# Kernel tuning notes

Hardware: AMD Instinct MI355X
Metric: run time of the kernel (lower is better)

## Reference

```python
import jax, jax.numpy as jnp
import numpy as np
import math

B, S, D = 1, 2048, 2048
H, KVH = 16, 8
HD = D // H                      # 128
M_, N_ = 8, 256                  # S = M_*N_ blocks of tokens
FH = 5632                        # multiple_of-rounded int(2*(4*D)/3)
EPS = 1e-6
THETA = 10000.0


def rmsnorm(x, w, eps=EPS):
    xf = x.astype(jnp.float32)
    y = xf * jax.lax.rsqrt(jnp.mean(xf * xf, axis=-1, keepdims=True) + eps)
    return y.astype(x.dtype) * w


def apply_rope(x, cos, sin):
    # x: (B, S, h, HD); cos/sin: (S, HD//2) -- consecutive-pair complex rotation
    x2 = x.reshape(*x.shape[:-1], HD // 2, 2)
    xr, xi = x2[..., 0], x2[..., 1]
    c = cos[None, :, None, :]
    s = sin[None, :, None, :]
    out = jnp.stack([xr * c - xi * s, xr * s + xi * c], axis=-1)
    return out.reshape(x.shape)


def setup_inputs() -> dict:
    key = jax.random.key(0)
    ks = jax.random.split(key, 12)
    sc = 0.02
    x = jax.random.normal(ks[0], (B, S, D), jnp.float32)
    vec = jax.random.normal(ks[1], (B, M_, D), jnp.float32)
    wq = jax.random.normal(ks[2], (D, H * HD), jnp.float32) * sc
    wk = jax.random.normal(ks[3], (D, KVH * HD), jnp.float32) * sc
    wv = jax.random.normal(ks[4], (D, KVH * HD), jnp.float32) * sc
    wo = jax.random.normal(ks[5], (H * HD, D), jnp.float32) * sc
    w1 = jax.random.normal(ks[6], (D, FH), jnp.float32) * sc
    w2 = jax.random.normal(ks[7], (FH, D), jnp.float32) * sc
    w3 = jax.random.normal(ks[8], (D, FH), jnp.float32) * sc
    mod_w = jax.random.normal(ks[9], (D, 3 * D), jnp.float32) * sc
    mod_b = jnp.zeros((3 * D,), jnp.float32)
    attn_norm_w = jnp.ones((D,), jnp.float32)
    ffn_norm_w = jnp.ones((D,), jnp.float32)
    # RoPE tables
    inv = 1.0 / (THETA ** (jnp.arange(0, HD, 2, dtype=jnp.float32) / HD))
    t = jnp.arange(S, dtype=jnp.float32)
    f = jnp.outer(t, inv)                      # (S, HD//2)
    cos, sin = jnp.cos(f), jnp.sin(f)
    mask = jnp.triu(jnp.full((S, S), -1e9, jnp.float32), 1)
    return dict(x=x, vec=vec, cos=cos, sin=sin, mask=mask, wq=wq, wk=wk, wv=wv,
                wo=wo, w1=w1, w2=w2, w3=w3, mod_w=mod_w, mod_b=mod_b,
                attn_norm_w=attn_norm_w, ffn_norm_w=ffn_norm_w)


def reference(x, vec, cos, sin, mask, wq, wk, wv, wo, w1, w2, w3,
              mod_w, mod_b, attn_norm_w, ffn_norm_w):
    n_rep = H // KVH
    # Modulation from per-block vectors (B, M, D) -> expand over N tokens/block
    mod = jax.nn.silu(vec) @ mod_w + mod_b
    shift, scale, gate = jnp.split(mod, 3, axis=-1)
    expand = lambda t: jnp.repeat(t, N_, axis=1)      # (B, M, D) -> (B, S, D)
    # Attention branch with modulated RMSNorm input
    h = rmsnorm(x, attn_norm_w)
    h = (1.0 + expand(scale)) * h + expand(shift)
    q = (h @ wq).reshape(B, S, H, HD)
    k = (h @ wk).reshape(B, S, KVH, HD)
    v = (h @ wv).reshape(B, S, KVH, HD)
    q = apply_rope(q, cos, sin)
    k = apply_rope(k, cos, sin)
    k = jnp.repeat(k, n_rep, axis=2)                  # repeat_kv
    v = jnp.repeat(v, n_rep, axis=2)
    scores = jnp.einsum('bshd,bthd->bhst', q, k) / math.sqrt(HD) + mask
    attn = jax.nn.softmax(scores.astype(jnp.float32), axis=-1).astype(q.dtype)
    o = jnp.einsum('bhst,bthd->bshd', attn, v).reshape(B, S, H * HD) @ wo
    x = x + expand(gate) * o
    # SwiGLU FFN branch
    hn = rmsnorm(x, ffn_norm_w)
    ff = (jax.nn.silu(hn @ w1) * (hn @ w3)) @ w2
    return x + ff
```

## Files before the change

kernel.cpp:

```cpp
#include <hip/hip_runtime.h>
#include <hip/hip_bf16.h>


typedef __attribute__((ext_vector_type(8))) short short8;
typedef __attribute__((ext_vector_type(4))) float f32x4;
typedef __attribute__((ext_vector_type(16))) float f32x16;
typedef __attribute__((ext_vector_type(4))) unsigned short u16x4;

#define MFMA16(a, b, c) __builtin_amdgcn_mfma_f32_16x16x32_bf16((a), (b), (c), 0, 0, 0)
#define MFMA32(a, b, c) __builtin_amdgcn_mfma_f32_32x32x16_bf16((a), (b), (c), 0, 0, 0)

__device__ __forceinline__ unsigned short f2b_bits(float f) {
    union { float f; unsigned int u; } cv; cv.f = f;
    unsigned int u = cv.u;
    u += 0x7fffu + ((u >> 16) & 1u);
    return (unsigned short)(u >> 16);
}
__device__ __forceinline__ float b2f_bits(unsigned short b) {
    union { float f; unsigned int u; } cv; cv.u = ((unsigned int)b) << 16; return cv.f;
}
__device__ __forceinline__ float silu_f(float x) { return x / (1.0f + __expf(-x)); }

__device__ __forceinline__ void async_copy16(const unsigned short* g, unsigned short* l) {
    __builtin_amdgcn_global_load_lds(
        (const __attribute__((address_space(1))) unsigned int*)g,
        (__attribute__((address_space(3))) unsigned int*)l, 16, 0, 0);
}

__global__ __launch_bounds__(256) void transpose_kernel(
    const float* __restrict__ W, unsigned short* __restrict__ WT, int K, int N,
    float scale)
{
    __shared__ float t[64][65];
    const int tid = threadIdx.x;
    const int k0 = blockIdx.y * 64, n0 = blockIdx.x * 64;
    {
        const int row = tid >> 2, cq = (tid & 3) * 16;
        const float* src = W + (size_t)(k0 + row) * N + n0 + cq;
        #pragma unroll
        for (int i = 0; i < 4; i++) {
            float4 v = *(const float4*)(src + i * 4);
            t[row][cq + i * 4 + 0] = v.x;
            t[row][cq + i * 4 + 1] = v.y;
            t[row][cq + i * 4 + 2] = v.z;
            t[row][cq + i * 4 + 3] = v.w;
        }
    }
    __syncthreads();
    {
        const int n = tid >> 2, kq = (tid & 3) * 16;
        short8 v0, v1;
        #pragma unroll
        for (int i = 0; i < 8; i++) {
            v0[i] = (short)f2b_bits(t[kq + i][n] * scale);
            v1[i] = (short)f2b_bits(t[kq + 8 + i][n] * scale);
        }
        unsigned short* dst = WT + (size_t)(n0 + n) * K + k0 + kq;
        *(short8*)(dst) = v0;
        *(short8*)(dst + 8) = v1;
    }
}

__global__ void silu_kernel(const float* __restrict__ in, float* __restrict__ outp, int n) {
    int i = blockIdx.x * 256 + threadIdx.x;
    if (i < n) outp[i] = silu_f(in[i]);
}

__global__ __launch_bounds__(256) void mod_gemm1(
    const float* __restrict__ svec, const float* __restrict__ mw,
    float* __restrict__ part)
{
    __shared__ float svs[8][256];
    const int tid = threadIdx.x;
    const int nb = blockIdx.x, kc = blockIdx.y;
    const int n = nb * 256 + tid;
    #pragma unroll
    for (int m8 = 0; m8 < 8; m8++) svs[m8][tid] = svec[m8 * 2048 + kc * 256 + tid];
    __syncthreads();
    float acc[8];
    #pragma unroll
    for (int m = 0; m < 8; m++) acc[m] = 0.0f;
    for (int k = 0; k < 256; k++) {
        const float w = mw[(size_t)(kc * 256 + k) * 6144 + n];
        #pragma unroll
        for (int m = 0; m < 8; m++) acc[m] += svs[m][k] * w;
    }
    #pragma unroll
    for (int m = 0; m < 8; m++) part[(size_t)(kc * 8 + m) * 6144 + n] = acc[m];
}

__global__ void mod_gemm2(const float* __restrict__ part, const float* __restrict__ mb,
                          float* __restrict__ modb)
{
    const int i = blockIdx.x * 256 + threadIdx.x;
    const int n = i % 6144;
    float a = mb[n];
    #pragma unroll
    for (int kc = 0; kc < 8; kc++) a += part[(size_t)(kc * 8 + (i / 6144)) * 6144 + n];
    modb[i] = a;
}

template<bool MOD>
__global__ __launch_bounds__(256) void norm_kernel(
    const float* __restrict__ xin, const float* __restrict__ w,
    const float* __restrict__ mod, unsigned short* __restrict__ outp)
{
    const int s = blockIdx.x, tid = threadIdx.x;
    const float* xr = xin + (size_t)s * 2048;
    float4 a4 = *(const float4*)(xr + tid * 8);
    float4 b4 = *(const float4*)(xr + tid * 8 + 4);
    float v[8] = {a4.x, a4.y, a4.z, a4.w, b4.x, b4.y, b4.z, b4.w};
    float ss = 0.0f;
    #pragma unroll
    for (int i = 0; i < 8; i++) ss += v[i] * v[i];
    #pragma unroll
    for (int off = 1; off < 64; off <<= 1) ss += __shfl_xor(ss, off);
    __shared__ float red[4];
    if ((tid & 63) == 0) red[tid >> 6] = ss;
    __syncthreads();
    ss = red[0] + red[1] + red[2] + red[3];
    const float inv = rsqrtf(ss * (1.0f / 2048.0f) + 1e-6f);
    const int g = s >> 8;
    #pragma unroll
    for (int i = 0; i < 8; i++) {
        const int d = tid * 8 + i;
        float y = v[i] * inv * w[d];
        if (MOD) y = y * (1.0f + mod[g * 6144 + 2048 + d]) + mod[g * 6144 + d];
        outp[(size_t)s * 2048 + d] = f2b_bits(y);
    }
}

enum { EP_QKV = 0, EP_BF16 = 1, EP_SILUMUL = 2, EP_PART = 3 };

template<int EPI>
__global__ __launch_bounds__(256, 2) void gemm_kernel(
    const unsigned short* __restrict__ A, const unsigned short* __restrict__ BT,
    void* __restrict__ outp, void* __restrict__ outp2, void* __restrict__ outp3,
    const unsigned short* __restrict__ up,
    const float* __restrict__ ct, const float* __restrict__ st,
    int M, int N, int K, int kspl)
{
    __shared__ unsigned short As[8192];
    __shared__ unsigned short Bs[8192];
    const int tid = threadIdx.x;
    const int lane = tid & 63, wave = tid >> 6;

    const int nwg = gridDim.x * gridDim.y;
    const int fid = blockIdx.y * gridDim.x + blockIdx.x;
    const int sid = (fid & 7) * (nwg >> 3) + (fid >> 3);
    const int m0 = (sid / gridDim.x) * 128;
    const int n0 = (sid % gridDim.x) * 128;
    const int kb0 = blockIdx.z * kspl;

    const int wr = (wave >> 1) * 64, wc = (wave & 1) * 64;
    const int lr = lane & 15, lg = lane >> 4;
    const int rcol = (lg ^ ((lr >> 1) & 3)) * 8;

    const int cl0 = (wave * 2 + 0) * 64 + lane;
    const int cl1 = (wave * 2 + 1) * 64 + lane;
    const int r0 = cl0 >> 2, c0 = cl0 & 3;
    const int r1 = cl1 >> 2, c1 = cl1 & 3;
    const unsigned short* gA0 = A + (size_t)(m0 + r0) * K + kb0 + (c0 ^ ((r0 >> 1) & 3)) * 8;
    const unsigned short* gA1 = A + (size_t)(m0 + r1) * K + kb0 + (c1 ^ ((r1 >> 1) & 3)) * 8;
    const unsigned short* gB0 = BT + (size_t)(n0 + r0) * K + kb0 + (c0 ^ ((r0 >> 1) & 3)) * 8;
    const unsigned short* gB1 = BT + (size_t)(n0 + r1) * K + kb0 + (c1 ^ ((r1 >> 1) & 3)) * 8;

    f32x4 acc[4][4];
    #pragma unroll
    for (int i = 0; i < 4; i++)
        #pragma unroll
        for (int j = 0; j < 4; j++) acc[i][j] = (f32x4){0.f, 0.f, 0.f, 0.f};

    const int nsteps = kspl >> 5;

    auto stage = [&](int buf, int kofs) {
        unsigned short* la = As + buf * 4096 + wave * 1024;
        unsigned short* lb = Bs + buf * 4096 + wave * 1024;
        async_copy16(gA0 + kofs, la);
        async_copy16(gA1 + kofs, la + 512);
        async_copy16(gB0 + kofs, lb);
        async_copy16(gB1 + kofs, lb + 512);
    };
    auto dostep = [&](int t, int cur) {
        if (t + 1 < nsteps) stage(cur ^ 1, (t + 1) * 32);
        const unsigned short* ab = As + cur * 4096;
        const unsigned short* bb = Bs + cur * 4096;
        short8 af[4], bfr[4];
        #pragma unroll
        for (int i = 0; i < 4; i++)
            af[i] = *(const short8*)&ab[(wr + i * 16 + lr) * 32 + rcol];
        #pragma unroll
        for (int j = 0; j < 4; j++)
            bfr[j] = *(const short8*)&bb[(wc + j * 16 + lr) * 32 + rcol];
        #pragma unroll
        for (int i = 0; i < 4; i++)
            #pragma unroll
            for (int j = 0; j < 4; j++)
                acc[i][j] = MFMA16(af[i], bfr[j], acc[i][j]);
        __syncthreads();
    };

    stage(0, 0);
    __syncthreads();
    for (int t = 0; t < nsteps; t += 2) { dostep(t, 0); dostep(t + 1, 1); }

    #pragma unroll
    for (int i = 0; i < 4; i++) {
        #pragma unroll
        for (int j = 0; j < 4; j++) {
            const int rb = m0 + wr + i * 16 + lg * 4;
            const int c  = n0 + wc + j * 16 + lr;
            if constexpr (EPI == EP_QKV) {
                if (n0 < 3072) {
                    const int crel = (n0 < 2048) ? c : (c - 2048);
                    const int dd = crel & 127;
                    const int pr = dd >> 1;
                    #pragma unroll
                    for (int r = 0; r < 4; r++) {
                        const float v = acc[i][j][r];
                        const float p = __shfl_xor(v, 1);
                        const float cs = ct[(rb + r) * 64 + pr];
                        const float sn = st[(rb + r) * 64 + pr];
                        const float res = (dd & 1) ? (p * sn + v * cs) : (v * cs - p * sn);
                        if (n0 < 2048)
                            ((unsigned short*)outp)[(size_t)(rb + r) * 2048 + crel] = f2b_bits(res);
                        else
                            ((unsigned short*)outp2)[(size_t)(rb + r) * 1024 + crel] = f2b_bits(res);
                    }
                } else {
                    u16x4 pk4;
                    #pragma unroll
                    for (int r = 0; r < 4; r++) pk4[r] = f2b_bits(acc[i][j][r]);
                    *(u16x4*)((unsigned short*)outp3 + (size_t)(c - 3072) * 2048 + rb) = pk4;
                }
            } else if constexpr (EPI == EP_PART) {
                float* pout = (float*)outp + (size_t)blockIdx.z * M * N;
                #pragma unroll
                for (int r = 0; r < 4; r++)
                    pout[(size_t)(rb + r) * N + c] = acc[i][j][r];
            } else {
                #pragma unroll
                for (int r = 0; r < 4; r++) {
                    const size_t idx = (size_t)(rb + r) * N + c;
                    if constexpr (EPI == EP_BF16) {
                        ((unsigned short*)outp)[idx] = f2b_bits(acc[i][j][r]);
                    } else {
                        const float uu = b2f_bits(up[idx]);
                        ((unsigned short*)outp)[idx] = f2b_bits(silu_f(uu) * acc[i][j][r]);
                    }
                }
            }
        }
    }
}

__global__ void combine_xgate(const float* __restrict__ p, const float* __restrict__ x,
                              const float* __restrict__ modp, float* __restrict__ out)
{
    const size_t i = ((size_t)blockIdx.x * 256 + threadIdx.x) * 4;
    const int row = (int)(i >> 11), col = (int)(i & 2047);
    const float4 a = *(const float4*)(p + i);
    const float4 b = *(const float4*)(p + (size_t)2048 * 2048 + i);
    const float4 xv = *(const float4*)(x + i);
    const float4 g = *(const float4*)(modp + (row >> 8) * 6144 + 4096 + col);
    float4 o;
    o.x = xv.x + g.x * (a.x + b.x);
    o.y = xv.y + g.y * (a.y + b.y);
    o.z = xv.z + g.z * (a.z + b.z);
    o.w = xv.w + g.w * (a.w + b.w);
    *(float4*)(out + i) = o;
}

__global__ void combine_w2(const float* __restrict__ p, float* __restrict__ out)
{
    const size_t i = ((size_t)blockIdx.x * 256 + threadIdx.x) * 4;
    const float4 a = *(const float4*)(p + i);
    const float4 b = *(const float4*)(p + (size_t)2048 * 2048 + i);
    float4 o = *(const float4*)(out + i);
    o.x += a.x + b.x; o.y += a.y + b.y; o.z += a.z + b.z; o.w += a.w + b.w;
    *(float4*)(out + i) = o;
}

__global__ __launch_bounds__(256, 2) void attn_kernel(
    const unsigned short* __restrict__ q,
    const unsigned short* __restrict__ kk,
    const unsigned short* __restrict__ vT,
    unsigned short* __restrict__ o)
{
    __shared__ unsigned short Ks[2][8192];
    __shared__ unsigned short Vs[2][8192];
    const int tid = threadIdx.x, wave = tid >> 6, lane = tid & 63;
    const int l5 = lane & 31, hi = lane >> 5;
    const int kvh = blockIdx.x;
    const int qt  = 63 - blockIdx.y;
    const int hs = wave >> 1, ks = wave & 1;
    const int h = kvh * 2 + hs;
    const int q0 = qt * 32;
    const int qrow = q0 + l5;
    const int niter = (qt >> 1) + 1;
    const int nss = (niter + 1) >> 1;

    short8 qf[8];
    {
        const unsigned short* qp = q + (size_t)qrow * 2048 + h * 128 + hi * 8;
        #pragma unroll
        for (int kf = 0; kf < 8; kf++) qf[kf] = *(const short8*)(qp + kf * 16);
    }

    f32x16 ot[4];
    #pragma unroll
    for (int df = 0; df < 4; df++)
        #pragma unroll
        for (int r = 0; r < 16; r++) ot[df][r] = 0.0f;
    float m_ = -3e30f, l_ = 0.0f;

    for (int ss = 0; ss < nss; ss++) {
        const int kvA = ss * 128;
        #pragma unroll
        for (int t = 0; t < 2; t++) {
            #pragma unroll
            for (int i = 0; i < 4; i++) {
                const int cl = (wave * 4 + i) * 64 + lane;
                const int row = cl >> 4, c = cl & 15;
                async_copy16(kk + (size_t)(kvA + t * 64 + row) * 1024 + kvh * 128
                                 + ((c ^ (row & 15)) * 8),
                             &Ks[t][(wave * 4 + i) * 512]);
            }
            #pragma unroll
            for (int i = 0; i < 4; i++) {
                const int cl = (wave * 4 + i) * 64 + lane;
                const int row = cl >> 3, c = cl & 7;
                async_copy16(vT + (size_t)(kvh * 128 + row) * 2048 + kvA + t * 64
                                 + ((c ^ (row & 7)) * 8),
                             &Vs[t][(wave * 4 + i) * 512]);
            }
        }
        __syncthreads();

        const int j = 2 * ss + ks;
        if (j < niter) {
            const int kv0 = j * 64;
            f32x16 st_[2];
            #pragma unroll
            for (int nf = 0; nf < 2; nf++)
                #pragma unroll
                for (int r = 0; r < 16; r++) st_[nf][r] = 0.0f;
            #pragma unroll
            for (int kf = 0; kf < 8; kf++) {
                const int ch = (kf * 2 + hi) ^ (l5 & 15);
                const short8 k0v = *(const short8*)&Ks[ks][l5 * 128 + ch * 8];
                const short8 k1v = *(const short8*)&Ks[ks][(l5 + 32) * 128 + ch * 8];
                st_[0] = MFMA32(k0v, qf[kf], st_[0]);
                st_[1] = MFMA32(k1v, qf[kf], st_[1]);
            }
            float sv[2][16];
            #pragma unroll
            for (int nf = 0; nf < 2; nf++)
                #pragma unroll
                for (int r = 0; r < 16; r++) {
                    const int kvi = kv0 + nf * 32 + (r & 3) + 8 * (r >> 2) + 4 * hi;
                    sv[nf][r] = (kvi > qrow) ? -3e30f : st_[nf][r];
                }
            float pmax = sv[0][0];
            #pragma unroll
            for (int nf = 0; nf < 2; nf++)
                #pragma unroll
                for (int r = 0; r < 16; r++) pmax = fmaxf(pmax, sv[nf][r]);
            pmax = fmaxf(pmax, __shfl_xor(pmax, 32));
            const float mnew = fmaxf(m_, pmax);
            const float alpha = __expf(m_ - mnew);
            m_ = mnew;
            float rs = 0.0f;
            #pragma unroll
            for (int nf = 0; nf < 2; nf++)
                #pragma unroll
                for (int r = 0; r < 16; r++) {
                    const float p = __expf(sv[nf][r] - mnew);
                    sv[nf][r] = p;
                    rs += p;
                }
            rs += __shfl_xor(rs, 32);
            l_ = l_ * alpha + rs;
            #pragma unroll
            for (int df = 0; df < 4; df++)
                #pragma unroll
                for (int r = 0; r < 16; r++) ot[df][r] *= alpha;
            short8 pa[4];
            #pragma unroll
            for (int nf = 0; nf < 2; nf++) {
                #pragma unroll
                for (int hh = 0; hh < 2; hh++) {
                    unsigned int a0 = ((unsigned int)f2b_bits(sv[nf][8 * hh + 1]) << 16) | f2b_bits(sv[nf][8 * hh + 0]);
                    unsigned int a1 = ((unsigned int)f2b_bits(sv[nf][8 * hh + 3]) << 16) | f2b_bits(sv[nf][8 * hh + 2]);
                    unsigned int a2 = ((unsigned int)f2b_bits(sv[nf][8 * hh + 5]) << 16) | f2b_bits(sv[nf][8 * hh + 4]);
                    unsigned int a3 = ((unsigned int)f2b_bits(sv[nf][8 * hh + 7]) << 16) | f2b_bits(sv[nf][8 * hh + 6]);
                    const unsigned int x0 = (unsigned int)__shfl_xor((int)a0, 32);
                    const unsigned int x1 = (unsigned int)__shfl_xor((int)a1, 32);
                    const unsigned int x2 = (unsigned int)__shfl_xor((int)a2, 32);
                    const unsigned int x3 = (unsigned int)__shfl_xor((int)a3, 32);
                    union { unsigned int u[4]; short8 s; } cv;
                    cv.u[0] = hi ? x2 : a0;
                    cv.u[1] = hi ? x3 : a1;
                    cv.u[2] = hi ? a2 : x0;
                    cv.u[3] = hi ? a3 : x1;
                    pa[nf * 2 + hh] = cv.s;
                }
            }
            #pragma unroll
            for (int df = 0; df < 4; df++) {
                const int d = df * 32 + l5;
                #pragma unroll
                for (int kvf = 0; kvf < 4; kvf++) {
                    const int ch = (kvf * 2 + hi) ^ (d & 7);
                    const short8 vfrag = *(const short8*)&Vs[ks][d * 64 + ch * 8];
                    ot[df] = MFMA32(vfrag, pa[kvf], ot[df]);
                }
            }
        }
        __syncthreads();
    }

    float* Osh = (float*)&Ks[0][0];
    float* msh = (float*)&Vs[0][0];
    if (ks == 1) {
        #pragma unroll
        for (int df = 0; df < 4; df++)
            #pragma unroll
            for (int r = 0; r < 16; r++) {
                const int d = df * 32 + (r & 3) + 8 * (r >> 2) + 4 * hi;
                Osh[hs * 4096 + d * 32 + l5] = ot[df][r];
            }
        if (hi == 0) { msh[hs * 64 + l5] = m_; msh[hs * 64 + 32 + l5] = l_; }
    }
    __syncthreads();
    if (ks == 0) {
        const float m1 = msh[hs * 64 + l5], l1 = msh[hs * 64 + 32 + l5];
        const float mF = fmaxf(m_, m1);
        const float a0 = __expf(m_ - mF), a1 = __expf(m1 - mF);
        const float rinv = 1.0f / (l_ * a0 + l1 * a1);
        #pragma unroll
        for (int df = 0; df < 4; df++) {
            #pragma unroll
            for (int g = 0; g < 4; g++) {
                u16x4 pk;
                #pragma unroll
                for (int e = 0; e < 4; e++) {
                    const int d = df * 32 + e + 8 * g + 4 * hi;
                    const float ov = ot[df][4 * g + e] * a0 + Osh[hs * 4096 + d * 32 + l5] * a1;
                    pk[e] = f2b_bits(ov * rinv);
                }
                *(u16x4*)(o + (size_t)qrow * 2048 + h * 128 + df * 32 + 8 * g + 4 * hi) = pk;
            }
        }
    }
}

extern "C" void kernel_launch(void* const* d_in, const int* in_sizes, int n_in,
                              void* d_out, int out_size, void* d_ws, size_t ws_size,
                              hipStream_t stream) {
    (void)in_sizes; (void)n_in; (void)out_size; (void)ws_size;
    const float* x     = (const float*)d_in[0];
    const float* vec   = (const float*)d_in[1];
    const float* cosb  = (const float*)d_in[2];
    const float* sinb  = (const float*)d_in[3];
    const float* wq    = (const float*)d_in[5];
    const float* wk    = (const float*)d_in[6];
    const float* wv    = (const float*)d_in[7];
    const float* wo    = (const float*)d_in[8];
    const float* w1    = (const float*)d_in[9];
    const float* w2    = (const float*)d_in[10];
    const float* w3    = (const float*)d_in[11];
    const float* mod_w = (const float*)d_in[12];
    const float* mod_b = (const float*)d_in[13];
    const float* anw   = (const float*)d_in[14];
    const float* fnw   = (const float*)d_in[15];
    float* out = (float*)d_out;

    char* ws = (char*)d_ws;
    size_t off = 0;
    auto alloc = [&](size_t bytes) -> void* {
        void* p = ws + off; off += (bytes + 255) & ~(size_t)255; return p;
    };
    unsigned short* WTqkv = (unsigned short*)alloc((size_t)4096 * 2048 * 2);
    unsigned short* WTo   = (unsigned short*)alloc((size_t)2048 * 2048 * 2);
    unsigned short* WT1   = (unsigned short*)alloc((size_t)5632 * 2048 * 2);
    unsigned short* WT3   = (unsigned short*)alloc((size_t)5632 * 2048 * 2);
    unsigned short* WT2   = (unsigned short*)alloc((size_t)2048 * 5632 * 2);
    float* svec = (float*)alloc((size_t)8 * 2048 * 4);
    float* part = (float*)alloc((size_t)64 * 6144 * 4);
    float* modb = (float*)alloc((size_t)8 * 6144 * 4);
    unsigned short* h    = (unsigned short*)alloc((size_t)2048 * 2048 * 2);
    unsigned short* qb   = (unsigned short*)alloc((size_t)2048 * 2048 * 2);
    unsigned short* kb   = (unsigned short*)alloc((size_t)2048 * 1024 * 2);
    unsigned short* vT   = (unsigned short*)alloc((size_t)1024 * 2048 * 2);
    unsigned short* ob   = (unsigned short*)alloc((size_t)2048 * 2048 * 2);
    unsigned short* u    = (unsigned short*)alloc((size_t)2048 * 5632 * 2);
    unsigned short* ffin = (unsigned short*)alloc((size_t)2048 * 5632 * 2);

    float* pxg = (float*)u;
    float* pw2 = (float*)h;

    const float qscale = 0.08838834764831845f;

    transpose_kernel<<<dim3(32, 32), 256, 0, stream>>>(wq, WTqkv, 2048, 2048, qscale);
    transpose_kernel<<<dim3(16, 32), 256, 0, stream>>>(wk, WTqkv + (size_t)2048 * 2048, 2048, 1024, 1.0f);
    transpose_kernel<<<dim3(16, 32), 256, 0, stream>>>(wv, WTqkv + (size_t)3072 * 2048, 2048, 1024, 1.0f);
    transpose_kernel<<<dim3(32, 32), 256, 0, stream>>>(wo, WTo, 2048, 2048, 1.0f);
    transpose_kernel<<<dim3(88, 32), 256, 0, stream>>>(w1, WT1, 2048, 5632, 1.0f);
    transpose_kernel<<<dim3(88, 32), 256, 0, stream>>>(w3, WT3, 2048, 5632, 1.0f);
    transpose_kernel<<<dim3(32, 88), 256, 0, stream>>>(w2, WT2, 5632, 2048, 1.0f);

    silu_kernel<<<64, 256, 0, stream>>>(vec, svec, 8 * 2048);
    mod_gemm1<<<dim3(24, 8), 256, 0, stream>>>(svec, mod_w, part);
    mod_gemm2<<<192, 256, 0, stream>>>(part, mod_b, modb);

    norm_kernel<true><<<2048, 256, 0, stream>>>(x, anw, modb, h);

    gemm_kernel<EP_QKV><<<dim3(32, 16), 256, 0, stream>>>(
        h, WTqkv, qb, kb, vT, nullptr, cosb, sinb, 2048, 4096, 2048, 2048);

    attn_kernel<<<dim3(8, 64), 256, 0, stream>>>(qb, kb, vT, ob);

    gemm_kernel<EP_PART><<<dim3(16, 16, 2), 256, 0, stream>>>(
        ob, WTo, pxg, nullptr, nullptr, nullptr, nullptr, nullptr, 2048, 2048, 2048, 1024);
    combine_xgate<<<4096, 256, 0, stream>>>(pxg, x, modb, out);

    norm_kernel<false><<<2048, 256, 0, stream>>>(out, fnw, nullptr, h);

    gemm_kernel<EP_BF16><<<dim3(44, 16), 256, 0, stream>>>(
        h, WT1, u, nullptr, nullptr, nullptr, nullptr, nullptr, 2048, 5632, 2048, 2048);
    gemm_kernel<EP_SILUMUL><<<dim3(44, 16), 256, 0, stream>>>(
        h, WT3, ffin, nullptr, nullptr, u, nullptr, nullptr, 2048, 5632, 2048, 2048);

    gemm_kernel<EP_PART><<<dim3(16, 16, 2), 256, 0, stream>>>(
        ffin, WT2, pw2, nullptr, nullptr, nullptr, nullptr, nullptr, 2048, 2048, 5632, 2816);
    combine_w2<<<4096, 256, 0, stream>>>(pw2, out);
}
```

Baseline: 460.2 us.

## Deepen GEMM LDS pipeline to four stages and restructure attention work split

The GEMM kernel moves from a double buffer to a four-deep LDS ring with three tiles in flight. It uses explicit vmcnt waits, raw s_barrier and setprio around the MFMA block, so global-to-LDS latency overlaps more compute and the per-step full sync is lighter. The attention kernel drops the KV split across wave pairs and its cross-wave LDS merge. Instead each block handles a 64-row query slab, with the two wave pairs on different 32-row halves sharing double-buffered K/V tiles, and the grid is halved. The trade-off is doubled GEMM LDS use, which may limit occupancy, and fewer attention blocks with longer serial KV loops.

New measurement: 507.6 us. 10.3% more time.

```diff
diff --git a/kernel.cpp b/kernel.cpp
--- a/kernel.cpp
+++ b/kernel.cpp
@@ -9,6 +9,7 @@
 
 #define MFMA16(a, b, c) __builtin_amdgcn_mfma_f32_16x16x32_bf16((a), (b), (c), 0, 0, 0)
 #define MFMA32(a, b, c) __builtin_amdgcn_mfma_f32_32x32x16_bf16((a), (b), (c), 0, 0, 0)
+#define VMCNT(n) asm volatile("s_waitcnt vmcnt(" #n ")" ::: "memory")
 
 __device__ __forceinline__ unsigned short f2b_bits(float f) {
     union { float f; unsigned int u; } cv; cv.f = f;
@@ -140,8 +141,8 @@
     const float* __restrict__ ct, const float* __restrict__ st,
     int M, int N, int K, int kspl)
 {
-    __shared__ unsigned short As[8192];
-    __shared__ unsigned short Bs[8192];
+    __shared__ unsigned short As[4 * 4096];
+    __shared__ unsigned short Bs[4 * 4096];
     const int tid = threadIdx.x;
     const int lane = tid & 63, wave = tid >> 6;
 
@@ -171,20 +172,28 @@
         #pragma unroll
         for (int j = 0; j < 4; j++) acc[i][j] = (f32x4){0.f, 0.f, 0.f, 0.f};
 
-    const int nsteps = kspl >> 5;
-
-    auto stage = [&](int buf, int kofs) {
-        unsigned short* la = As + buf * 4096 + wave * 1024;
-        unsigned short* lb = Bs + buf * 4096 + wave * 1024;
-        async_copy16(gA0 + kofs, la);
-        async_copy16(gA1 + kofs, la + 512);
-        async_copy16(gB0 + kofs, lb);
-        async_copy16(gB1 + kofs, lb + 512);
+    const int nt = kspl >> 5;
+
+    auto stagef = [&](int t) {
+        const int b = t & 3;
+        const int ko = t * 32;
+        unsigned short* la = As + b * 4096 + wave * 1024;
+        unsigned short* lb = Bs + b * 4096 + wave * 1024;
+        async_copy16(gA0 + ko, la);
+        async_copy16(gA1 + ko, la + 512);
+        async_copy16(gB0 + ko, lb);
+        async_copy16(gB1 + ko, lb + 512);
     };
-    auto dostep = [&](int t, int cur) {
-        if (t + 1 < nsteps) stage(cur ^ 1, (t + 1) * 32);
-        const unsigned short* ab = As + cur * 4096;
-        const unsigned short* bb = Bs + cur * 4096;
+
+    stagef(0); stagef(1); stagef(2);
+    VMCNT(8);
+    __builtin_amdgcn_sched_barrier(0);
+    __builtin_amdgcn_s_barrier();
+    __builtin_amdgcn_sched_barrier(0);
+
+    for (int t = 0; t < nt; ++t) {
+        const unsigned short* ab = As + (t & 3) * 4096;
+        const unsigned short* bb = Bs + (t & 3) * 4096;
         short8 af[4], bfr[4];
         #pragma unroll
         for (int i = 0; i < 4; i++)
@@ -192,17 +201,24 @@
         #pragma unroll
         for (int j = 0; j < 4; j++)
             bfr[j] = *(const short8*)&bb[(wc + j * 16 + lr) * 32 + rcol];
+        if (t + 3 < nt) stagef(t + 3);
+        __builtin_amdgcn_s_setprio(1);
         #pragma unroll
         for (int i = 0; i < 4; i++)
             #pragma unroll
             for (int j = 0; j < 4; j++)
                 acc[i][j] = MFMA16(af[i], bfr[j], acc[i][j]);
-        __syncthreads();
-    };
-
-    stage(0, 0);
-    __syncthreads();
-    for (int t = 0; t < nsteps; t += 2) { dostep(t, 0); dostep(t + 1, 1); }
+        __builtin_amdgcn_s_setprio(0);
+        const int rem = nt - 1 - t;
+        if (rem >= 3)      { VMCNT(8); }
+        else if (rem == 2) { VMCNT(4); }
+        else if (rem == 1) { VMCNT(0); }
+        __builtin_amdgcn_sched_barrier(0);
+        if (rem > 0) {
+            __builtin_amdgcn_s_barrier();
+            __builtin_amdgcn_sched_barrier(0);
+        }
+    }
 
     #pragma unroll
     for (int i = 0; i < 4; i++) {
@@ -292,13 +308,11 @@
     const int tid = threadIdx.x, wave = tid >> 6, lane = tid & 63;
     const int l5 = lane & 31, hi = lane >> 5;
     const int kvh = blockIdx.x;
-    const int qt  = 63 - blockIdx.y;
-    const int hs = wave >> 1, ks = wave & 1;
+    const int slab = 31 - blockIdx.y;
+    const int hs = wave >> 1, qs = wave & 1;
     const int h = kvh * 2 + hs;
-    const int q0 = qt * 32;
-    const int qrow = q0 + l5;
-    const int niter = (qt >> 1) + 1;
-    const int nss = (niter + 1) >> 1;
+    const int qrow = slab * 64 + qs * 32 + l5;
+    const int ntiles = slab + 1;
 
     short8 qf[8];
     {
@@ -314,143 +328,121 @@
         for (int r = 0; r < 16; r++) ot[df][r] = 0.0f;
     float m_ = -3e30f, l_ = 0.0f;
 
-    for (int ss = 0; ss < nss; ss++) {
-        const int kvA = ss * 128;
-        #pragma unroll
-        for (int t = 0; t < 2; t++) {
-            #pragma unroll
-            for (int i = 0; i < 4; i++) {
-                const int cl = (wave * 4 + i) * 64 + lane;
-                const int row = cl >> 4, c = cl & 15;
-                async_copy16(kk + (size_t)(kvA + t * 64 + row) * 1024 + kvh * 128
-                                 + ((c ^ (row & 15)) * 8),
-                             &Ks[t][(wave * 4 + i) * 512]);
+    auto stage = [&](int j, int b) {
+        #pragma unroll
+        for (int i = 0; i < 4; i++) {
+            const int cl = (wave * 4 + i) * 64 + lane;
+            const int row = cl >> 4, c = cl & 15;
+            async_copy16(kk + (size_t)(j * 64 + row) * 1024 + kvh * 128
+                             + ((c ^ (row & 15)) * 8),
+                         &Ks[b][(wave * 4 + i) * 512]);
+        }
+        #pragma unroll
+        for (int i = 0; i < 4; i++) {
+            const int cl = (wave * 4 + i) * 64 + lane;
+            const int row = cl >> 3, c = cl & 7;
+            async_copy16(vT + (size_t)(kvh * 128 + row) * 2048 + j * 64
+                             + ((c ^ (row & 7)) * 8),
+                         &Vs[b][(wave * 4 + i) * 512]);
+        }
+    };
+
+    stage(0, 0);
+    __syncthreads();
+
+    for (int j = 0; j < ntiles; ++j) {
+        const int buf = j & 1;
+        if (j + 1 < ntiles) stage(j + 1, buf ^ 1);
+        const int kv0 = j * 64;
+        f32x16 st_[2];
+        #pragma unroll
+        for (int nf = 0; nf < 2; nf++)
+            #pragma unroll
+            for (int r = 0; r < 16; r++) st_[nf][r] = 0.0f;
+        #pragma unroll
+        for (int kf = 0; kf < 8; kf++) {
+            const int ch = (kf * 2 + hi) ^ (l5 & 15);
+            const short8 k0v = *(const short8*)&Ks[buf][l5 * 128 + ch * 8];
+            const short8 k1v = *(const short8*)&Ks[buf][(l5 + 32) * 128 + ch * 8];
+            st_[0] = MFMA32(k0v, qf[kf], st_[0]);
+            st_[1] = MFMA32(k1v, qf[kf], st_[1]);
+        }
+        float sv[2][16];
+        #pragma unroll
+        for (int nf = 0; nf < 2; nf++)
+            #pragma unroll
+            for (int r = 0; r < 16; r++) {
+                const int kvi = kv0 + nf * 32 + (r & 3) + 8 * (r >> 2) + 4 * hi;
+                sv[nf][r] = (kvi > qrow) ? -3e30f : st_[nf][r];
             }
-            #pragma unroll
-            for (int i = 0; i < 4; i++) {
-                const int cl = (wave * 4 + i) * 64 + lane;
-                const int row = cl >> 3, c = cl & 7;
-                async_copy16(vT + (size_t)(kvh * 128 + row) * 2048 + kvA + t * 64
-                                 + ((c ^ (row & 7)) * 8),
-                             &Vs[t][(wave * 4 + i) * 512]);
+        float pmax = sv[0][0];
+        #pragma unroll
+        for (int nf = 0; nf < 2; nf++)
+            #pragma unroll
+            for (int r = 0; r < 16; r++) pmax = fmaxf(pmax, sv[nf][r]);
+        pmax = fmaxf(pmax, __shfl_xor(pmax, 32));
+        const float mnew = fmaxf(m_, pmax);
+        const float alpha = __expf(m_ - mnew);
+        m_ = mnew;
+        float rs = 0.0f;
+        #pragma unroll
+        for (int nf = 0; nf < 2; nf++)
+            #pragma unroll
+            for (int r = 0; r < 16; r++) {
+                const float p = __expf(sv[nf][r] - mnew);
+                sv[nf][r] = p;
+                rs += p;
             }
+        rs += __shfl_xor(rs, 32);
+        l_ = l_ * alpha + rs;
+        #pragma unroll
+        for (int df = 0; df < 4; df++)
+            #pragma unroll
+            for (int r = 0; r < 16; r++) ot[df][r] *= alpha;
+        short8 pa[4];
+        #pragma unroll
+        for (int nf = 0; nf < 2; nf++) {
+            #pragma unroll
+            for (int hh = 0; hh < 2; hh++) {
+                unsigned int a0 = ((unsigned int)f2b_bits(sv[nf][8 * hh + 1]) << 16) | f2b_bits(sv[nf][8 * hh + 0]);
+                unsigned int a1 = ((unsigned int)f2b_bits(sv[nf][8 * hh + 3]) << 16) | f2b_bits(sv[nf][8 * hh + 2]);
+                unsigned int a2 = ((unsigned int)f2b_bits(sv[nf][8 * hh + 5]) << 16) | f2b_bits(sv[nf][8 * hh + 4]);
+                unsigned int a3 = ((unsigned int)f2b_bits(sv[nf][8 * hh + 7]) << 16) | f2b_bits(sv[nf][8 * hh + 6]);
+                const unsigned int x0 = (unsigned int)__shfl_xor((int)a0, 32);
+                const unsigned int x1 = (unsigned int)__shfl_xor((int)a1, 32);
+                const unsigned int x2 = (unsigned int)__shfl_xor((int)a2, 32);
+                const unsigned int x3 = (unsigned int)__shfl_xor((int)a3, 32);
+                union { unsigned int u[4]; short8 s; } cv;
+                cv.u[0] = hi ? x2 : a0;
+                cv.u[1] = hi ? x3 : a1;
+                cv.u[2] = hi ? a2 : x0;
+                cv.u[3] = hi ? a3 : x1;
+                pa[nf * 2 + hh] = cv.s;
+            }
+        }
+        #pragma unroll
+        for (int df = 0; df < 4; df++) {
+            const int d = df * 32 + l5;
+            #pragma unroll
+            for (int kvf = 0; kvf < 4; kvf++) {
+                const int ch = (kvf * 2 + hi) ^ (d & 7);
+                const short8 vfrag = *(const short8*)&Vs[buf][d * 64 + ch * 8];
+                ot[df] = MFMA32(vfrag, pa[kvf], ot[df]);
+            }
         }
         __syncthreads();
-
-        const int j = 2 * ss + ks;
-        if (j < niter) {
-            const int kv0 = j * 64;
-            f32x16 st_[2];
-            #pragma unroll
-            for (int nf = 0; nf < 2; nf++)
-                #pragma unroll
-                for (int r = 0; r < 16; r++) st_[nf][r] = 0.0f;
-            #pragma unroll
-            for (int kf = 0; kf < 8; kf++) {
-                const int ch = (kf * 2 + hi) ^ (l5 & 15);
-                const short8 k0v = *(const short8*)&Ks[ks][l5 * 128 + ch * 8];
-                const short8 k1v = *(const short8*)&Ks[ks][(l5 + 32) * 128 + ch * 8];
-                st_[0] = MFMA32(k0v, qf[kf], st_[0]);
-                st_[1] = MFMA32(k1v, qf[kf], st_[1]);
-            }
-            float sv[2][16];
-            #pragma unroll
-            for (int nf = 0; nf < 2; nf++)
-                #pragma unroll
-                for (int r = 0; r < 16; r++) {
-                    const int kvi = kv0 + nf * 32 + (r & 3) + 8 * (r >> 2) + 4 * hi;
-                    sv[nf][r] = (kvi > qrow) ? -3e30f : st_[nf][r];
-                }
-            float pmax = sv[0][0];
-            #pragma unroll
-            for (int nf = 0; nf < 2; nf++)
-                #pragma unroll
-                for (int r = 0; r < 16; r++) pmax = fmaxf(pmax, sv[nf][r]);
-            pmax = fmaxf(pmax, __shfl_xor(pmax, 32));
-            const float mnew = fmaxf(m_, pmax);
-            const float alpha = __expf(m_ - mnew);
-            m_ = mnew;
-            float rs = 0.0f;
-            #pragma unroll
-            for (int nf = 0; nf < 2; nf++)
-                #pragma unroll
-                for (int r = 0; r < 16; r++) {
-                    const float p = __expf(sv[nf][r] - mnew);
-                    sv[nf][r] = p;
-                    rs += p;
-                }
-            rs += __shfl_xor(rs, 32);
-            l_ = l_ * alpha + rs;
-            #pragma unroll
-            for (int df = 0; df < 4; df++)
-                #pragma unroll
-                for (int r = 0; r < 16; r++) ot[df][r] *= alpha;
-            short8 pa[4];
-            #pragma unroll
-            for (int nf = 0; nf < 2; nf++) {
-                #pragma unroll
-                for (int hh = 0; hh < 2; hh++) {
-                    unsigned int a0 = ((unsigned int)f2b_bits(sv[nf][8 * hh + 1]) << 16) | f2b_bits(sv[nf][8 * hh + 0]);
-                    unsigned int a1 = ((unsigned int)f2b_bits(sv[nf][8 * hh + 3]) << 16) | f2b_bits(sv[nf][8 * hh + 2]);
-                    unsigned int a2 = ((unsigned int)f2b_bits(sv[nf][8 * hh + 5]) << 16) | f2b_bits(sv[nf][8 * hh + 4]);
-                    unsigned int a3 = ((unsigned int)f2b_bits(sv[nf][8 * hh + 7]) << 16) | f2b_bits(sv[nf][8 * hh + 6]);
-                    const unsigned int x0 = (unsigned int)__shfl_xor((int)a0, 32);
-                    const unsigned int x1 = (unsigned int)__shfl_xor((int)a1, 32);
-                    const unsigned int x2 = (unsigned int)__shfl_xor((int)a2, 32);
-                    const unsigned int x3 = (unsigned int)__shfl_xor((int)a3, 32);
-                    union { unsigned int u[4]; short8 s; } cv;
-                    cv.u[0] = hi ? x2 : a0;
-                    cv.u[1] = hi ? x3 : a1;
-                    cv.u[2] = hi ? a2 : x0;
-                    cv.u[3] = hi ? a3 : x1;
-                    pa[nf * 2 + hh] = cv.s;
-                }
-            }
-            #pragma unroll
-            for (int df = 0; df < 4; df++) {
-                const int d = df * 32 + l5;
-                #pragma unroll
-                for (int kvf = 0; kvf < 4; kvf++) {
-                    const int ch = (kvf * 2 + hi) ^ (d & 7);
-                    const short8 vfrag = *(const short8*)&Vs[ks][d * 64 + ch * 8];
-                    ot[df] = MFMA32(vfrag, pa[kvf], ot[df]);
-                }
-            }
-        }
-        __syncthreads();
-    }
-
-    float* Osh = (float*)&Ks[0][0];
-    float* msh = (float*)&Vs[0][0];
-    if (ks == 1) {
-        #pragma unroll
-        for (int df = 0; df < 4; df++)
-            #pragma unroll
-            for (int r = 0; r < 16; r++) {
-                const int d = df * 32 + (r & 3) + 8 * (r >> 2) + 4 * hi;
-                Osh[hs * 4096 + d * 32 + l5] = ot[df][r];
-            }
-        if (hi == 0) { msh[hs * 64 + l5] = m_; msh[hs * 64 + 32 + l5] = l_; }
-    }
-    __syncthreads();
-    if (ks == 0) {
-        const float m1 = msh[hs * 64 + l5], l1 = msh[hs * 64 + 32 + l5];
-        const float mF = fmaxf(m_, m1);
-        const float a0 = __expf(m_ - mF), a1 = __expf(m1 - mF);
-        const float rinv = 1.0f / (l_ * a0 + l1 * a1);
-        #pragma unroll
-        for (int df = 0; df < 4; df++) {
-            #pragma unroll
-            for (int g = 0; g < 4; g++) {
-                u16x4 pk;
-                #pragma unroll
-                for (int e = 0; e < 4; e++) {
-                    const int d = df * 32 + e + 8 * g + 4 * hi;
-                    const float ov = ot[df][4 * g + e] * a0 + Osh[hs * 4096 + d * 32 + l5] * a1;
-                    pk[e] = f2b_bits(ov * rinv);
-                }
-                *(u16x4*)(o + (size_t)qrow * 2048 + h * 128 + df * 32 + 8 * g + 4 * hi) = pk;
-            }
+    }
+
+    const float rinv = 1.0f / l_;
+    #pragma unroll
+    for (int df = 0; df < 4; df++) {
+        #pragma unroll
+        for (int g = 0; g < 4; g++) {
+            u16x4 pk;
+            #pragma unroll
+            for (int e = 0; e < 4; e++)
+                pk[e] = f2b_bits(ot[df][4 * g + e] * rinv);
+            *(u16x4*)(o + (size_t)qrow * 2048 + h * 128 + df * 32 + 8 * g + 4 * hi) = pk;
         }
     }
 }
@@ -519,7 +511,7 @@
     gemm_kernel<EP_QKV><<<dim3(32, 16), 256, 0, stream>>>(
         h, WTqkv, qb, kb, vT, nullptr, cosb, sinb, 2048, 4096, 2048, 2048);
 
-    attn_kernel<<<dim3(8, 64), 256, 0, stream>>>(qb, kb, vT, ob);
+    attn_kernel<<<dim3(8, 32), 256, 0, stream>>>(qb, kb, vT, ob);
 
     gemm_kernel<EP_PART><<<dim3(16, 16, 2), 256, 0, stream>>>(
         ob, WTo, pxg, nullptr, nullptr, nullptr, nullptr, nullptr, 2048, 2048, 2048, 1024);
```

## Fuse w1/w3 into one interleaved GEMM with 256x256 tiles and split-K

Applied to the files above, without the earlier changes.

Adds an 8-wave GEMM kernel with 256x256 tiles, 128 KB of dynamic LDS and a finely interleaved load/compute schedule using barriers, setprio and explicit vmcnt waits. It is used for the output projection, the FFN up-projection and the down-projection. The w1 and w3 weights are transposed into one buffer with their columns interleaved in groups of 8. That lets a single GEMM compute both products and apply silu(a)*b in the epilogue through a lane shuffle, so the bf16 intermediate no longer makes a round trip through memory. The w2 GEMM now splits K three ways, and the combine kernel sums three partials. The cost is extra fp32 partial traffic, and one workgroup per CU at 512 threads, which lowers occupancy.

Measured after the change: 468.3 us. No clear change (+1.7%).

```diff
diff --git a/kernel.cpp b/kernel.cpp
--- a/kernel.cpp
+++ b/kernel.cpp
@@ -9,6 +9,7 @@
 
 #define MFMA16(a, b, c) __builtin_amdgcn_mfma_f32_16x16x32_bf16((a), (b), (c), 0, 0, 0)
 #define MFMA32(a, b, c) __builtin_amdgcn_mfma_f32_32x32x16_bf16((a), (b), (c), 0, 0, 0)
+#define VMCNT(n) asm volatile("s_waitcnt vmcnt(" #n ")" ::: "memory")
 
 __device__ __forceinline__ unsigned short f2b_bits(float f) {
     union { float f; unsigned int u; } cv; cv.f = f;
@@ -61,9 +62,49 @@
     }
 }
 
+__global__ __launch_bounds__(256) void transpose_w13_kernel(
+    const float* __restrict__ W1, const float* __restrict__ W3,
+    unsigned short* __restrict__ WT, int K, int N)
+{
+    __shared__ float t[64][65];
+    const int tid = threadIdx.x;
+    const int k0 = blockIdx.y * 64, n0 = blockIdx.x * 64;
+    for (int which = 0; which < 2; which++) {
+        const float* W = which ? W3 : W1;
+        __syncthreads();
+        {
+            const int row = tid >> 2, cq = (tid & 3) * 16;
+            const float* src = W + (size_t)(k0 + row) * N + n0 + cq;
+            #pragma unroll
+            for (int i = 0; i < 4; i++) {
+                float4 v = *(const float4*)(src + i * 4);
+                t[row][cq + i * 4 + 0] = v.x;
+                t[row][cq + i * 4 + 1] = v.y;
+                t[row][cq + i * 4 + 2] = v.z;
+                t[row][cq + i * 4 + 3] = v.w;
+            }
+        }
+        __syncthreads();
+        {
+            const int n = tid >> 2, kq = (tid & 3) * 16;
+            short8 v0, v1;
+            #pragma unroll
+            for (int i = 0; i < 8; i++) {
+                v0[i] = (short)f2b_bits(t[kq + i][n]);
+                v1[i] = (short)f2b_bits(t[kq + 8 + i][n]);
+            }
+            const int ngl = n0 + n;
+            const int r = ((ngl >> 3) << 4) + (ngl & 7) + which * 8;
+            unsigned short* dst = WT + (size_t)r * K + k0 + kq;
+            *(short8*)(dst) = v0;
+            *(short8*)(dst + 8) = v1;
+        }
+    }
+}
+
 __global__ void silu_kernel(const float* __restrict__ in, float* __restrict__ outp, int n) {
     int i = blockIdx.x * 256 + threadIdx.x;
-    if (i < n) outp[i] = silu_f(in[i]);
+    if (i < n) outp[i] = silu_f(i < n ? in[i] : 0.0f);
 }
 
 __global__ __launch_bounds__(256) void mod_gemm1(
@@ -130,15 +171,14 @@
     }
 }
 
-enum { EP_QKV = 0, EP_BF16 = 1, EP_SILUMUL = 2, EP_PART = 3 };
+enum { EP_QKV = 0 };
 
 template<int EPI>
 __global__ __launch_bounds__(256, 2) void gemm_kernel(
     const unsigned short* __restrict__ A, const unsigned short* __restrict__ BT,
     void* __restrict__ outp, void* __restrict__ outp2, void* __restrict__ outp3,
-    const unsigned short* __restrict__ up,
     const float* __restrict__ ct, const float* __restrict__ st,
-    int M, int N, int K, int kspl)
+    int M, int N, int K)
 {
     __shared__ unsigned short As[8192];
     __shared__ unsigned short Bs[8192];
@@ -150,7 +190,6 @@
     const int sid = (fid & 7) * (nwg >> 3) + (fid >> 3);
     const int m0 = (sid / gridDim.x) * 128;
     const int n0 = (sid % gridDim.x) * 128;
-    const int kb0 = blockIdx.z * kspl;
 
     const int wr = (wave >> 1) * 64, wc = (wave & 1) * 64;
     const int lr = lane & 15, lg = lane >> 4;
@@ -160,10 +199,10 @@
     const int cl1 = (wave * 2 + 1) * 64 + lane;
     const int r0 = cl0 >> 2, c0 = cl0 & 3;
     const int r1 = cl1 >> 2, c1 = cl1 & 3;
-    const unsigned short* gA0 = A + (size_t)(m0 + r0) * K + kb0 + (c0 ^ ((r0 >> 1) & 3)) * 8;
-    const unsigned short* gA1 = A + (size_t)(m0 + r1) * K + kb0 + (c1 ^ ((r1 >> 1) & 3)) * 8;
-    const unsigned short* gB0 = BT + (size_t)(n0 + r0) * K + kb0 + (c0 ^ ((r0 >> 1) & 3)) * 8;
-    const unsigned short* gB1 = BT + (size_t)(n0 + r1) * K + kb0 + (c1 ^ ((r1 >> 1) & 3)) * 8;
+    const unsigned short* gA0 = A + (size_t)(m0 + r0) * K + (c0 ^ ((r0 >> 1) & 3)) * 8;
+    const unsigned short* gA1 = A + (size_t)(m0 + r1) * K + (c1 ^ ((r1 >> 1) & 3)) * 8;
+    const unsigned short* gB0 = BT + (size_t)(n0 + r0) * K + (c0 ^ ((r0 >> 1) & 3)) * 8;
+    const unsigned short* gB1 = BT + (size_t)(n0 + r1) * K + (c1 ^ ((r1 >> 1) & 3)) * 8;
 
     f32x4 acc[4][4];
     #pragma unroll
@@ -171,7 +210,7 @@
         #pragma unroll
         for (int j = 0; j < 4; j++) acc[i][j] = (f32x4){0.f, 0.f, 0.f, 0.f};
 
-    const int nsteps = kspl >> 5;
+    const int nsteps = K >> 5;
 
     auto stage = [&](int buf, int kofs) {
         unsigned short* la = As + buf * 4096 + wave * 1024;
@@ -210,45 +249,172 @@
         for (int j = 0; j < 4; j++) {
             const int rb = m0 + wr + i * 16 + lg * 4;
             const int c  = n0 + wc + j * 16 + lr;
-            if constexpr (EPI == EP_QKV) {
-                if (n0 < 3072) {
-                    const int crel = (n0 < 2048) ? c : (c - 2048);
-                    const int dd = crel & 127;
-                    const int pr = dd >> 1;
-                    #pragma unroll
-                    for (int r = 0; r < 4; r++) {
-                        const float v = acc[i][j][r];
-                        const float p = __shfl_xor(v, 1);
-                        const float cs = ct[(rb + r) * 64 + pr];
-                        const float sn = st[(rb + r) * 64 + pr];
-                        const float res = (dd & 1) ? (p * sn + v * cs) : (v * cs - p * sn);
-                        if (n0 < 2048)
-                            ((unsigned short*)outp)[(size_t)(rb + r) * 2048 + crel] = f2b_bits(res);
-                        else
-                            ((unsigned short*)outp2)[(size_t)(rb + r) * 1024 + crel] = f2b_bits(res);
-                    }
-                } else {
-                    u16x4 pk4;
-                    #pragma unroll
-                    for (int r = 0; r < 4; r++) pk4[r] = f2b_bits(acc[i][j][r]);
-                    *(u16x4*)((unsigned short*)outp3 + (size_t)(c - 3072) * 2048 + rb) = pk4;
+            if (n0 < 3072) {
+                const int crel = (n0 < 2048) ? c : (c - 2048);
+                const int dd = crel & 127;
+                const int pr = dd >> 1;
+                #pragma unroll
+                for (int r = 0; r < 4; r++) {
+                    const float v = acc[i][j][r];
+                    const float p = __shfl_xor(v, 1);
+                    const float cs = ct[(rb + r) * 64 + pr];
+                    const float sn = st[(rb + r) * 64 + pr];
+                    const float res = (dd & 1) ? (p * sn + v * cs) : (v * cs - p * sn);
+                    if (n0 < 2048)
+                        ((unsigned short*)outp)[(size_t)(rb + r) * 2048 + crel] = f2b_bits(res);
+                    else
+                        ((unsigned short*)outp2)[(size_t)(rb + r) * 1024 + crel] = f2b_bits(res);
                 }
-            } else if constexpr (EPI == EP_PART) {
-                float* pout = (float*)outp + (size_t)blockIdx.z * M * N;
+            } else {
+                u16x4 pk4;
+                #pragma unroll
+                for (int r = 0; r < 4; r++) pk4[r] = f2b_bits(acc[i][j][r]);
+                *(u16x4*)((unsigned short*)outp3 + (size_t)(c - 3072) * 2048 + rb) = pk4;
+            }
+        }
+    }
+}
+
+enum { G_SILU = 0, G_PART = 1 };
+
+template<int EPI>
+__global__ __launch_bounds__(512, 1) void gemm256_kernel(
+    const unsigned short* __restrict__ A, const unsigned short* __restrict__ BT,
+    void* __restrict__ outp, int M, int N, int Nout, int K, int ktiles, int nsplit)
+{
+    extern __shared__ unsigned short smem[];
+    unsigned short* As_ = smem;
+    unsigned short* Bs_ = smem + 2 * 16384;
+    const int tid = threadIdx.x;
+    const int lane = tid & 63, wid = tid >> 6;
+    const int wm = wid >> 2, wn = wid & 3;
+    const int lr = lane & 15, lg = lane >> 4;
+
+    const int nwg = gridDim.x * gridDim.y;
+    const int fid = blockIdx.y * gridDim.x + blockIdx.x;
+    const int sid = (fid & 7) * (nwg >> 3) + (fid >> 3);
+    const int m0 = (sid / gridDim.x) * 256;
+    const int n0 = (sid % gridDim.x) * 256;
+    const int z = blockIdx.z;
+    const int kt0 = (z * ktiles) / nsplit;
+    const int nt = ((z + 1) * ktiles) / nsplit - kt0;
+
+    const int srow8 = wid * 8 + (lane >> 3);
+    const int schunk = lane & 7;
+
+    f32x4 acc[8][4];
+    #pragma unroll
+    for (int i = 0; i < 8; i++)
+        #pragma unroll
+        for (int j = 0; j < 4; j++) acc[i][j] = (f32x4){0.f, 0.f, 0.f, 0.f};
+
+    auto stageA = [&](int u, int t) {
+        const int row = u * 64 + srow8;
+        async_copy16(A + (size_t)(m0 + row) * K + (size_t)(kt0 + t) * 64
+                       + ((schunk ^ (row & 7)) << 3),
+                     As_ + (t & 1) * 16384 + (u * 64 + wid * 8) * 64);
+    };
+    auto stageB = [&](int u, int t) {
+        const int row = u * 64 + srow8;
+        async_copy16(BT + (size_t)(n0 + row) * K + (size_t)(kt0 + t) * 64
+                       + ((schunk ^ (row & 7)) << 3),
+                     Bs_ + (t & 1) * 16384 + (u * 64 + wid * 8) * 64);
+    };
+
+    short8 areg[4], breg[2][4];
+    auto loadA = [&](const unsigned short* ab, int mh, int ks) {
+        #pragma unroll
+        for (int i = 0; i < 4; i++) {
+            const int row = wm * 128 + mh * 64 + i * 16 + lr;
+            areg[i] = *(const short8*)&ab[row * 64 + (((ks * 4 + lg) ^ (row & 7)) << 3)];
+        }
+    };
+    auto loadB = [&](const unsigned short* bb, int ks) {
+        #pragma unroll
+        for (int nj = 0; nj < 4; nj++) {
+            const int row = wn * 64 + nj * 16 + lr;
+            breg[ks][nj] = *(const short8*)&bb[row * 64 + (((ks * 4 + lg) ^ (row & 7)) << 3)];
+        }
+    };
+    auto mmac = [&](int mh, int ks) {
+        #pragma unroll
+        for (int i = 0; i < 4; i++)
+            #pragma unroll
+            for (int nj = 0; nj < 4; nj++)
+                acc[mh * 4 + i][nj] = MFMA16(areg[i], breg[ks][nj], acc[mh * 4 + i][nj]);
+    };
+
+    stageA(0, 0); stageA(2, 0);
+    stageB(0, 0); stageB(1, 0);
+    stageB(2, 0); stageB(3, 0);
+    stageA(1, 0); stageA(3, 0);
+    VMCNT(2);
+    __builtin_amdgcn_sched_barrier(0);
+    __builtin_amdgcn_s_barrier();
+    __builtin_amdgcn_sched_barrier(0);
+
+    for (int t = 0; t < nt; ++t) {
+        const unsigned short* ab = As_ + (t & 1) * 16384;
+        const unsigned short* bb = Bs_ + (t & 1) * 16384;
+        const bool more = (t + 1 < nt);
+        loadB(bb, 0);
+        loadA(ab, 0, 0);
+        if (more) { stageA(0, t + 1); stageA(2, t + 1); }
+        __builtin_amdgcn_s_barrier();
+        __builtin_amdgcn_s_setprio(1);
+        mmac(0, 0);
+        __builtin_amdgcn_s_setprio(0);
+        __builtin_amdgcn_s_barrier();
+        loadB(bb, 1);
+        loadA(ab, 0, 1);
+        if (more) { stageB(0, t + 1); stageB(1, t + 1); }
+        __builtin_amdgcn_s_barrier();
+        __builtin_amdgcn_s_setprio(1);
+        mmac(0, 1);
+        __builtin_amdgcn_s_setprio(0);
+        if (more) { VMCNT(4); } else { VMCNT(0); }
+        __builtin_amdgcn_sched_barrier(0);
+        __builtin_amdgcn_s_barrier();
+        __builtin_amdgcn_sched_barrier(0);
+        loadA(ab, 1, 0);
+        if (more) { stageB(2, t + 1); stageB(3, t + 1); }
+        __builtin_amdgcn_s_barrier();
+        __builtin_amdgcn_s_setprio(1);
+        mmac(1, 0);
+        __builtin_amdgcn_s_setprio(0);
+        __builtin_amdgcn_s_barrier();
+        loadA(ab, 1, 1);
+        if (more) { stageA(1, t + 1); stageA(3, t + 1); }
+        __builtin_amdgcn_s_barrier();
+        __builtin_amdgcn_s_setprio(1);
+        mmac(1, 1);
+        __builtin_amdgcn_s_setprio(0);
+        if (more) { VMCNT(2); __builtin_amdgcn_sched_barrier(0); }
+        __builtin_amdgcn_s_barrier();
+        __builtin_amdgcn_sched_barrier(0);
+    }
+
+    #pragma unroll
+    for (int mi = 0; mi < 8; mi++) {
+        #pragma unroll
+        for (int nj = 0; nj < 4; nj++) {
+            const int rb = m0 + wm * 128 + mi * 16 + lg * 4;
+            const int c  = n0 + wn * 64 + nj * 16 + lr;
+            if constexpr (EPI == G_SILU) {
+                const int oc = ((c - lr) >> 1) + lr;
+                #pragma unroll
+                for (int r = 0; r < 4; r++) {
+                    const float v = acc[mi][nj][r];
+                    const float p = __shfl_xor(v, 8);
+                    if (lr < 8)
+                        ((unsigned short*)outp)[(size_t)(rb + r) * Nout + oc] =
+                            f2b_bits(silu_f(v) * p);
+                }
+            } else {
+                float* pout = (float*)outp + (size_t)z * M * Nout;
                 #pragma unroll
                 for (int r = 0; r < 4; r++)
-                    pout[(size_t)(rb + r) * N + c] = acc[i][j][r];
-            } else {
-                #pragma unroll
-                for (int r = 0; r < 4; r++) {
-                    const size_t idx = (size_t)(rb + r) * N + c;
-                    if constexpr (EPI == EP_BF16) {
-                        ((unsigned short*)outp)[idx] = f2b_bits(acc[i][j][r]);
-                    } else {
-                        const float uu = b2f_bits(up[idx]);
-                        ((unsigned short*)outp)[idx] = f2b_bits(silu_f(uu) * acc[i][j][r]);
-                    }
-                }
+                    pout[(size_t)(rb + r) * Nout + c] = acc[mi][nj][r];
             }
         }
     }
@@ -276,8 +442,10 @@
     const size_t i = ((size_t)blockIdx.x * 256 + threadIdx.x) * 4;
     const float4 a = *(const float4*)(p + i);
     const float4 b = *(const float4*)(p + (size_t)2048 * 2048 + i);
+    const float4 c = *(const float4*)(p + (size_t)2 * 2048 * 2048 + i);
     float4 o = *(const float4*)(out + i);
-    o.x += a.x + b.x; o.y += a.y + b.y; o.z += a.z + b.z; o.w += a.w + b.w;
+    o.x += a.x + b.x + c.x; o.y += a.y + b.y + c.y;
+    o.z += a.z + b.z + c.z; o.w += a.w + b.w + c.w;
     *(float4*)(out + i) = o;
 }
 
@@ -483,8 +651,7 @@
     };
     unsigned short* WTqkv = (unsigned short*)alloc((size_t)4096 * 2048 * 2);
     unsigned short* WTo   = (unsigned short*)alloc((size_t)2048 * 2048 * 2);
-    unsigned short* WT1   = (unsigned short*)alloc((size_t)5632 * 2048 * 2);
-    unsigned short* WT3   = (unsigned short*)alloc((size_t)5632 * 2048 * 2);
+    unsigned short* WT13  = (unsigned short*)alloc((size_t)11264 * 2048 * 2);
     unsigned short* WT2   = (unsigned short*)alloc((size_t)2048 * 5632 * 2);
     float* svec = (float*)alloc((size_t)8 * 2048 * 4);
     float* part = (float*)alloc((size_t)64 * 6144 * 4);
@@ -502,12 +669,16 @@
 
     const float qscale = 0.08838834764831845f;
 
+    hipFuncSetAttribute((const void*)gemm256_kernel<G_SILU>,
+                        hipFuncAttributeMaxDynamicSharedMemorySize, 131072);
+    hipFuncSetAttribute((const void*)gemm256_kernel<G_PART>,
+                        hipFuncAttributeMaxDynamicSharedMemorySize, 131072);
+
     transpose_kernel<<<dim3(32, 32), 256, 0, stream>>>(wq, WTqkv, 2048, 2048, qscale);
     transpose_kernel<<<dim3(16, 32), 256, 0, stream>>>(wk, WTqkv + (size_t)2048 * 2048, 2048, 1024, 1.0f);
     transpose_kernel<<<dim3(16, 32), 256, 0, stream>>>(wv, WTqkv + (size_t)3072 * 2048, 2048, 1024, 1.0f);
     transpose_kernel<<<dim3(32, 32), 256, 0, stream>>>(wo, WTo, 2048, 2048, 1.0f);
-    transpose_kernel<<<dim3(88, 32), 256, 0, stream>>>(w1, WT1, 2048, 5632, 1.0f);
-    transpose_kernel<<<dim3(88, 32), 256, 0, stream>>>(w3, WT3, 2048, 5632, 1.0f);
+    transpose_w13_kernel<<<dim3(88, 32), 256, 0, stream>>>(w1, w3, WT13, 2048, 5632);
     transpose_kernel<<<dim3(32, 88), 256, 0, stream>>>(w2, WT2, 5632, 2048, 1.0f);
 
     silu_kernel<<<64, 256, 0, stream>>>(vec, svec, 8 * 2048);
@@ -517,22 +688,20 @@
     norm_kernel<true><<<2048, 256, 0, stream>>>(x, anw, modb, h);
 
     gemm_kernel<EP_QKV><<<dim3(32, 16), 256, 0, stream>>>(
-        h, WTqkv, qb, kb, vT, nullptr, cosb, sinb, 2048, 4096, 2048, 2048);
+        h, WTqkv, qb, kb, vT, cosb, sinb, 2048, 4096, 2048);
 
     attn_kernel<<<dim3(8, 64), 256, 0, stream>>>(qb, kb, vT, ob);
 
-    gemm_kernel<EP_PART><<<dim3(16, 16, 2), 256, 0, stream>>>(
-        ob, WTo, pxg, nullptr, nullptr, nullptr, nullptr, nullptr, 2048, 2048, 2048, 1024);
+    gemm256_kernel<G_PART><<<dim3(8, 8, 2), 512, 131072, stream>>>(
+        ob, WTo, pxg, 2048, 2048, 2048, 2048, 32, 2);
     combine_xgate<<<4096, 256, 0, stream>>>(pxg, x, modb, out);
 
     norm_kernel<false><<<2048, 256, 0, stream>>>(out, fnw, nullptr, h);
 
-    gemm_kernel<EP_BF16><<<dim3(44, 16), 256, 0, stream>>>(
-        h, WT1, u, nullptr, nullptr, nullptr, nullptr, nullptr, 2048, 5632, 2048, 2048);
-    gemm_kernel<EP_SILUMUL><<<dim3(44, 16), 256, 0, stream>>>(
-        h, WT3, ffin, nullptr, nullptr, u, nullptr, nullptr, 2048, 5632, 2048, 2048);
-
-    gemm_kernel<EP_PART><<<dim3(16, 16, 2), 256, 0, stream>>>(
-        ffin, WT2, pw2, nullptr, nullptr, nullptr, nullptr, nullptr, 2048, 2048, 5632, 2816);
+    gemm256_kernel<G_SILU><<<dim3(44, 8, 1), 512, 131072, stream>>>(
+        h, WT13, ffin, 2048, 11264, 5632, 2048, 32, 1);
+
+    gemm256_kernel<G_PART><<<dim3(8, 8, 3), 512, 131072, stream>>>(
+        ffin, WT2, pw2, 2048, 2048, 2048, 5632, 88, 3);
     combine_w2<<<4096, 256, 0, stream>>>(pw2, out);
 }
```
